# Optimization experiments

Measured on AMD Instinct MI355X. Metric: run time of the kernel, lower is better.

## Reference

```python
import jax, jax.numpy as jnp
import numpy as np

WS, SHIFT = 4, 2
Z, H, W = 16, 32, 32
C, HEADS, MLP = 384, 12, 1536
B = 4
N = WS ** 3                      # tokens per 3D window = 64
NW = (Z // WS) * (H // WS) * (W // WS)  # windows per sample = 256
L = Z * H * W
HEAD_DIM = C // HEADS


def _rel_pos_index():
    # replicates meshgrid_3d (which reverses its args) + index arithmetic
    arrs = (np.arange(WS), np.arange(WS), np.arange(WS))  # already symmetric (cubic)
    grids = []
    for i in range(3):
        slc = [1, 1, 1]; slc[i] = WS
        a = arrs[i].reshape(slc)
        for j in range(3):
            if j != i:
                a = a.repeat(WS, axis=j)
        grids.append(a)
    coords = np.stack(grids).reshape(3, -1)            # [3, N]
    rel = coords[:, :, None] - coords[:, None, :]      # [3, N, N]
    rel = rel.transpose(1, 2, 0)                       # [N, N, 3]
    rel[:, :, 0] += WS - 1
    rel[:, :, 1] += WS - 1
    rel[:, :, 2] += WS - 1
    rel[:, :, 0] *= (2 * WS - 1) * (2 * WS - 1)
    rel[:, :, 1] *= 2 * WS - 1
    return rel.sum(-1)                                 # [N, N] ints in [0, (2ws-1)^3)


def _attn_mask():
    # shifted-window mask, exactly as in build()
    m = np.zeros((Z, H, W))
    sl = (slice(0, -WS), slice(-WS, -SHIFT), slice(-SHIFT, None))
    cnt = 0
    for z in sl:
        for h in sl:
            for w in sl:
                m[z, h, w] = cnt
                cnt += 1
    mw = m.reshape(Z // WS, WS, H // WS, WS, W // WS, WS)
    mw = mw.transpose(0, 2, 4, 1, 3, 5).reshape(-1, N)        # [nW, N]
    diff = mw[:, None, :] - mw[:, :, None]                    # [nW, N, N]
    return np.where(diff != 0, -100.0, 0.0).astype(np.float32)


REL_IDX = jnp.asarray(_rel_pos_index())
MASK = jnp.asarray(_attn_mask())


def _ln(x, g, b):
    mu = jnp.mean(x, -1, keepdims=True)
    var = jnp.mean((x - mu) ** 2, -1, keepdims=True)
    return (x - mu) / jnp.sqrt(var + 1e-5) * g + b


def setup_inputs() -> dict:
    key = jax.random.key(0)
    ks = jax.random.split(key, 16)
    s = 0.02
    return {
        "x": jax.random.normal(ks[0], (B, L, C), jnp.float32),
        "norm1_g": jnp.ones((C,), jnp.float32),
        "norm1_b": jnp.zeros((C,), jnp.float32),
        "qkv_w": jax.random.normal(ks[1], (C, 3 * C), jnp.float32) * s,
        "qkv_b": jnp.zeros((3 * C,), jnp.float32),
        "proj_w": jax.random.normal(ks[2], (C, C), jnp.float32) * s,
        "proj_b": jnp.zeros((C,), jnp.float32),
        "rel_bias": jax.random.normal(ks[3], ((2 * WS - 1) ** 3, HEADS), jnp.float32) * s,
        "norm2_g": jnp.ones((C,), jnp.float32),
        "norm2_b": jnp.zeros((C,), jnp.float32),
        "fc1_w": jax.random.normal(ks[4], (C, MLP), jnp.float32) * s,
        "fc1_b": jnp.zeros((MLP,), jnp.float32),
        "fc2_w": jax.random.normal(ks[5], (MLP, C), jnp.float32) * s,
        "fc2_b": jnp.zeros((C,), jnp.float32),
    }


def reference(x, norm1_g, norm1_b, qkv_w, qkv_b, proj_w, proj_b, rel_bias,
              norm2_g, norm2_b, fc1_w, fc1_b, fc2_w, fc2_b):
    b = x.shape[0]
    skip = x
    h = _ln(x, norm1_g, norm1_b).reshape(b, Z, H, W, C)
    h = jnp.roll(h, (-SHIFT, -SHIFT, -SHIFT), axis=(1, 2, 3))
    # window partition -> [b*nW, N, C]
    win = h.reshape(b, Z // WS, WS, H // WS, WS, W // WS, WS, C)
    win = win.transpose(0, 1, 3, 5, 2, 4, 6, 7).reshape(-1, N, C)
    # windowed multi-head attention
    qkv = (win @ qkv_w + qkv_b).reshape(-1, N, 3, HEADS, HEAD_DIM)
    qkv = qkv.transpose(2, 0, 3, 1, 4)                        # [3, bnW, h, N, d]
    q, k, v = qkv[0], qkv[1], qkv[2]
    scale = HEAD_DIM ** -0.5
    attn = jnp.einsum('whnd,whmd->whnm', q * scale, k)        # [bnW, h, N, N]
    bias = rel_bias[REL_IDX.reshape(-1)].reshape(N, N, HEADS).transpose(2, 0, 1)
    attn = attn + bias[None]
    attn = attn.reshape(b, NW, HEADS, N, N) + MASK[None, :, None]
    attn = jax.nn.softmax(attn, axis=-1).reshape(-1, HEADS, N, N)
    o = jnp.einsum('whnm,whmd->whnd', attn, v)
    o = o.transpose(0, 2, 1, 3).reshape(-1, N, C) @ proj_w + proj_b
    # window reverse + unshift
    o = o.reshape(b, Z // WS, H // WS, W // WS, WS, WS, WS, C)
    o = o.transpose(0, 1, 4, 2, 5, 3, 6, 7).reshape(b, Z, H, W, C)
    o = jnp.roll(o, (SHIFT, SHIFT, SHIFT), axis=(1, 2, 3)).reshape(b, L, C)
    x2 = skip + o
    m = _ln(x2, norm2_g, norm2_b)
    m = jax.nn.gelu(m @ fc1_w + fc1_b, approximate=False) @ fc2_w + fc2_b
    return x2 + m
```

## Files before the change

### kernel.cpp

```cpp
#include <hip/hip_runtime.h>
#include <hip/hip_bf16.h>
#include <cstdint>
#include <cmath>


typedef __attribute__((ext_vector_type(4))) float f32x4;
typedef __attribute__((ext_vector_type(8))) __bf16 bf16x8_t;

static __device__ __forceinline__ short f2bf(float f) {
  unsigned u = __builtin_bit_cast(unsigned, f);
  unsigned lsb = (u >> 16) & 1u;
  u += 0x7fffu + lsb;
  return (short)(u >> 16);
}

static __device__ __forceinline__ void gload_lds16(const short* g, short* l) {
  __builtin_amdgcn_global_load_lds(
      (const __attribute__((address_space(1))) void*)g,
      (__attribute__((address_space(3))) void*)l, 16, 0, 0);
}

static constexpr size_t OFF_Q    = 0;
static constexpr size_t OFF_K    = 50331648;
static constexpr size_t OFF_V    = 100663296;
static constexpr size_t OFF_HID  = 0;
static constexpr size_t OFF_WIN  = 201326592;
static constexpr size_t OFF_WQ   = OFF_WIN + 50331648;
static constexpr size_t OFF_WP   = OFF_WQ  + 884736;
static constexpr size_t OFF_W1   = OFF_WP  + 294912;
static constexpr size_t OFF_W2   = OFF_W1  + 1179648;

__global__ void k_w2bf_t(const float* __restrict__ w, short* __restrict__ wt,
                         int K, int N) {
  int idx = blockIdx.x * 256 + threadIdx.x;
  if (idx >= K * N) return;
  int k = idx / N, n = idx - k * N;
  wt[(size_t)n * K + k] = f2bf(w[idx]);
}

__global__ __launch_bounds__(256) void k_ln1_window(
    const float* __restrict__ x, const float* __restrict__ gw,
    const float* __restrict__ gb, short* __restrict__ win) {
  int slot = blockIdx.x * 4 + (threadIdx.x >> 6);
  int lane = threadIdx.x & 63;
  int widx = slot >> 6, n = slot & 63;
  int bidx = widx >> 8, wloc = widx & 255;
  int z = ((wloc >> 6) << 2) + (n >> 4);
  int h = (((wloc >> 3) & 7) << 2) + ((n >> 2) & 3);
  int w = ((wloc & 7) << 2) + (n & 3);
  int zs = (z + 2) & 15, hs = (h + 2) & 31, ws = (w + 2) & 31;
  const float* xp = x + ((size_t)bidx * 16384 + zs * 1024 + hs * 32 + ws) * 384;
  float2 u[3]; float s = 0.f, s2 = 0.f;
#pragma unroll
  for (int j = 0; j < 3; j++) {
    u[j] = *(const float2*)(xp + lane * 2 + j * 128);
    s += u[j].x + u[j].y; s2 += u[j].x * u[j].x + u[j].y * u[j].y;
  }
#pragma unroll
  for (int o = 1; o < 64; o <<= 1) { s += __shfl_xor(s, o); s2 += __shfl_xor(s2, o); }
  float mu = s * (1.f / 384.f);
  float rinv = rsqrtf(s2 * (1.f / 384.f) - mu * mu + 1e-5f);
  short* wp = win + (size_t)slot * 384;
#pragma unroll
  for (int j = 0; j < 3; j++) {
    int c = lane * 2 + j * 128;
    ushort2 o;
    o.x = (unsigned short)f2bf((u[j].x - mu) * rinv * gw[c] + gb[c]);
    o.y = (unsigned short)f2bf((u[j].y - mu) * rinv * gw[c + 1] + gb[c + 1]);
    *(ushort2*)(wp + c) = o;
  }
}

__global__ __launch_bounds__(256) void k_ln2(
    const float* __restrict__ x2, const float* __restrict__ gw,
    const float* __restrict__ gb, short* __restrict__ h2) {
  int t = blockIdx.x * 4 + (threadIdx.x >> 6);
  int lane = threadIdx.x & 63;
  const float* xp = x2 + (size_t)t * 384;
  float2 u[3]; float s = 0.f, s2 = 0.f;
#pragma unroll
  for (int j = 0; j < 3; j++) {
    u[j] = *(const float2*)(xp + lane * 2 + j * 128);
    s += u[j].x + u[j].y; s2 += u[j].x * u[j].x + u[j].y * u[j].y;
  }
#pragma unroll
  for (int o = 1; o < 64; o <<= 1) { s += __shfl_xor(s, o); s2 += __shfl_xor(s2, o); }
  float mu = s * (1.f / 384.f);
  float rinv = rsqrtf(s2 * (1.f / 384.f) - mu * mu + 1e-5f);
  short* hp = h2 + (size_t)t * 384;
#pragma unroll
  for (int j = 0; j < 3; j++) {
    int c = lane * 2 + j * 128;
    ushort2 o;
    o.x = (unsigned short)f2bf((u[j].x - mu) * rinv * gw[c] + gb[c]);
    o.y = (unsigned short)f2bf((u[j].y - mu) * rinv * gw[c + 1] + gb[c + 1]);
    *(ushort2*)(hp + c) = o;
  }
}

template <int EPI, int KDIM>
__global__ __launch_bounds__(256) void k_gemm(
    const short* __restrict__ A, const short* __restrict__ Bt,
    const float* __restrict__ bias, short* __restrict__ ob0,
    short* __restrict__ ob1, short* __restrict__ ob2,
    const float* __restrict__ aux, float* __restrict__ of32) {
  __shared__ short As[16384];
  __shared__ short Bs[16384];
  const int tid = threadIdx.x;
  const int wave = tid >> 6, lane = tid & 63;
  const int g = lane >> 4, li = lane & 15;

  const int nx = gridDim.x;
  const int nwg = nx * gridDim.y;
  int bid = blockIdx.y * nx + blockIdx.x;
  const int cpx = nwg >> 3;
  bid = (bid & 7) * cpx + (bid >> 3);
  const int m0 = (bid / nx) << 7, n0 = (bid % nx) << 7;

  const int srow = tid >> 3;
  const int sc8 = (tid & 7) ^ (srow & 7);
  const short* gA = A + (size_t)(m0 + srow) * KDIM + sc8 * 8;
  const short* gB = Bt + (size_t)(n0 + srow) * KDIM + sc8 * 8;
  short* lA = As + wave * 512;
  short* lB = Bs + wave * 512;

  const int wm = wave >> 1, wn = wave & 1;
  const int kx = (li & 7) << 3;
  const short* ra = As + (wm * 64 + li) * 64;
  const short* rb = Bs + (wn * 64 + li) * 64;
  const int c00 = (g * 8) ^ kx;
  const int c32 = (32 + g * 8) ^ kx;

  f32x4 acc[4][4] = {};

#define STAGE(buf, kt)                                                        \
  do {                                                                        \
    _Pragma("unroll") for (int p = 0; p < 4; p++) {                           \
      gload_lds16(gA + (size_t)(p * 32) * KDIM + (kt),                        \
                  lA + (buf) * 8192 + p * 2048);                              \
      gload_lds16(gB + (size_t)(p * 32) * KDIM + (kt),                        \
                  lB + (buf) * 8192 + p * 2048);                              \
    }                                                                         \
  } while (0)

#define COMPUTE(buf)                                                          \
  do {                                                                        \
    const short* ra_ = ra + (buf) * 8192;                                     \
    const short* rb_ = rb + (buf) * 8192;                                     \
    bf16x8_t a0[4], a1[4], b0[4], b1[4];                                      \
    _Pragma("unroll") for (int i = 0; i < 4; i++) {                           \
      a0[i] = *(const bf16x8_t*)(ra_ + i * 1024 + c00);                       \
      a1[i] = *(const bf16x8_t*)(ra_ + i * 1024 + c32);                       \
      b0[i] = *(const bf16x8_t*)(rb_ + i * 1024 + c00);                       \
      b1[i] = *(const bf16x8_t*)(rb_ + i * 1024 + c32);                       \
    }                                                                         \
    _Pragma("unroll") for (int mi = 0; mi < 4; mi++)                          \
        _Pragma("unroll") for (int ni = 0; ni < 4; ni++) acc[mi][ni] =        \
        __builtin_amdgcn_mfma_f32_16x16x32_bf16(a0[mi], b0[ni], acc[mi][ni],  \
                                                0, 0, 0);                     \
    _Pragma("unroll") for (int mi = 0; mi < 4; mi++)                          \
        _Pragma("unroll") for (int ni = 0; ni < 4; ni++) acc[mi][ni] =        \
        __builtin_amdgcn_mfma_f32_16x16x32_bf16(a1[mi], b1[ni], acc[mi][ni],  \
                                                0, 0, 0);                     \
  } while (0)

  constexpr int NT = KDIM / 64;
  STAGE(0, 0);
  asm volatile("s_waitcnt vmcnt(0)" ::: "memory");
  __syncthreads();
  int cur = 0;
  for (int t = 0; t < NT - 1; ++t) {
    STAGE(cur ^ 1, (t + 1) * 64);
    COMPUTE(cur);
    asm volatile("s_waitcnt vmcnt(0)" ::: "memory");
    __syncthreads();
    cur ^= 1;
  }
  COMPUTE(cur);
#undef STAGE
#undef COMPUTE

#pragma unroll
  for (int mi = 0; mi < 4; mi++) {
#pragma unroll
    for (int ni = 0; ni < 4; ni++) {
      const int col = n0 + wn * 64 + ni * 16 + li;
      const float bc = bias[col];
      const int rbase = m0 + wm * 64 + mi * 16 + g * 4;
      if constexpr (EPI == 0) {
        const int s = col / 384;
        const int rem = col - s * 384;
        const int head = rem >> 5, d = rem & 31;
#pragma unroll
        for (int r = 0; r < 4; r++) {
          const int row = rbase + r;
          const int widx = row >> 6, n = row & 63;
          float v = acc[mi][ni][r] + bc;
          if (s == 0)
            ob0[(((size_t)widx * 12 + head) * 64 + n) * 32 + d] =
                f2bf(v * 0.17677669529663687f);
          else if (s == 1)
            ob1[(((size_t)widx * 12 + head) * 64 + n) * 32 + d] = f2bf(v);
          else
            ob2[(((size_t)widx * 12 + head) * 32 + d) * 64 + n] = f2bf(v);
        }
      } else if constexpr (EPI == 1) {
#pragma unroll
        for (int r = 0; r < 4; r++) {
          const int row = rbase + r;
          const int widx = row >> 6, n = row & 63;
          const int wloc = widx & 255, bb = widx >> 8;
          const int z = ((wloc >> 6) << 2) + (n >> 4);
          const int h = (((wloc >> 3) & 7) << 2) + ((n >> 2) & 3);
          const int w = ((wloc & 7) << 2) + (n & 3);
          const int zs = (z + 2) & 15, hs = (h + 2) & 31, wsx = (w + 2) & 31;
          const size_t t = (size_t)bb * 16384 + zs * 1024 + hs * 32 + wsx;
          of32[t * 384 + col] = aux[t * 384 + col] + acc[mi][ni][r] + bc;
        }
      } else if constexpr (EPI == 2) {
#pragma unroll
        for (int r = 0; r < 4; r++) {
          const int row = rbase + r;
          float v = acc[mi][ni][r] + bc;
          ob0[(size_t)row * 1536 + col] =
              f2bf(0.5f * v * (1.f + erff(v * 0.70710678118654752f)));
        }
      } else {
#pragma unroll
        for (int r = 0; r < 4; r++) {
          const int row = rbase + r;
          of32[(size_t)row * 384 + col] =
              aux[(size_t)row * 384 + col] + acc[mi][ni][r] + bc;
        }
      }
    }
  }
}

__global__ __launch_bounds__(256) void k_attn(
    const short* __restrict__ qb, const short* __restrict__ kb,
    const short* __restrict__ vb, const float* __restrict__ relb,
    short* __restrict__ owin) {
  __shared__ short pt[4][5120];
  const int wave = threadIdx.x >> 6;
  const int wh_ = blockIdx.x * 4 + wave;
  const int widx = wh_ / 12, head = wh_ - widx * 12;
  const int lane = threadIdx.x & 63;
  const int g = lane >> 4, li = lane & 15;
  const short* qp = qb + (size_t)wh_ * 2048;
  const short* kp = kb + (size_t)wh_ * 2048;
  const short* vp = vb + (size_t)wh_ * 2048;
  short* ptw = pt[wave];
  bf16x8_t kf[4], qf[4];
#pragma unroll
  for (int t = 0; t < 4; t++) {
    kf[t] = *(const bf16x8_t*)(kp + (t * 16 + li) * 32 + g * 8);
    qf[t] = *(const bf16x8_t*)(qp + (t * 16 + li) * 32 + g * 8);
  }
  f32x4 zero = {0.f, 0.f, 0.f, 0.f};
  f32x4 st[4][4];
#pragma unroll
  for (int ti = 0; ti < 4; ti++)
#pragma unroll
    for (int tj = 0; tj < 4; tj++)
      st[ti][tj] = __builtin_amdgcn_mfma_f32_16x16x32_bf16(kf[ti], qf[tj], zero, 0, 0, 0);
  const int wloc = widx & 255;
  const int wz = wloc >> 6, wh2 = (wloc >> 3) & 7, ww2 = wloc & 7;
#pragma unroll
  for (int tj = 0; tj < 4; tj++) {
    const int qn = tj * 16 + li;
    const int qz = qn >> 4, qh = (qn >> 2) & 3, qw = qn & 3;
    const int cq = ((wz < 3) ? 0 : ((qz < 2) ? 1 : 2)) * 9 +
                   ((wh2 < 7) ? 0 : ((qh < 2) ? 1 : 2)) * 3 +
                   ((ww2 < 7) ? 0 : ((qw < 2) ? 1 : 2));
    float mx = -1e30f;
#pragma unroll
    for (int ti = 0; ti < 4; ti++) {
#pragma unroll
      for (int r = 0; r < 4; r++) {
        const int kn = ti * 16 + g * 4 + r;
        const int kz = kn >> 4, kh = (kn >> 2) & 3, kw = kn & 3;
        const int ck = ((wz < 3) ? 0 : ((kz < 2) ? 1 : 2)) * 9 +
                       ((wh2 < 7) ? 0 : ((kh < 2) ? 1 : 2)) * 3 +
                       ((ww2 < 7) ? 0 : ((kw < 2) ? 1 : 2));
        const int idx = (qz - kz + 3) * 49 + (qh - kh + 3) * 7 + (qw - kw + 3);
        float v = st[ti][tj][r] + relb[idx * 12 + head] + ((ck == cq) ? 0.f : -100.f);
        st[ti][tj][r] = v;
        mx = fmaxf(mx, v);
      }
    }
    mx = fmaxf(mx, __shfl_xor(mx, 16));
    mx = fmaxf(mx, __shfl_xor(mx, 32));
    float sum = 0.f;
#pragma unroll
    for (int ti = 0; ti < 4; ti++)
#pragma unroll
      for (int r = 0; r < 4; r++) {
        float e = __expf(st[ti][tj][r] - mx);
        st[ti][tj][r] = e;
        sum += e;
      }
    sum += __shfl_xor(sum, 16);
    sum += __shfl_xor(sum, 32);
    const float rs = 1.f / sum;
#pragma unroll
    for (int ti = 0; ti < 4; ti++)
#pragma unroll
      for (int r = 0; r < 4; r++)
        ptw[qn * 80 + ti * 16 + g * 4 + r] = f2bf(st[ti][tj][r] * rs);
  }
  __syncthreads();
  f32x4 o[4][2] = {};
#pragma unroll
  for (int kb2 = 0; kb2 < 2; kb2++) {
    bf16x8_t pa[4], bv[2];
#pragma unroll
    for (int tq = 0; tq < 4; tq++)
      pa[tq] = *(const bf16x8_t*)(ptw + (tq * 16 + li) * 80 + kb2 * 32 + g * 8);
#pragma unroll
    for (int td = 0; td < 2; td++)
      bv[td] = *(const bf16x8_t*)(vp + (td * 16 + li) * 64 + kb2 * 32 + g * 8);
#pragma unroll
    for (int tq = 0; tq < 4; tq++)
#pragma unroll
      for (int td = 0; td < 2; td++)
        o[tq][td] = __builtin_amdgcn_mfma_f32_16x16x32_bf16(pa[tq], bv[td], o[tq][td], 0, 0, 0);
  }
#pragma unroll
  for (int tq = 0; tq < 4; tq++)
#pragma unroll
    for (int td = 0; td < 2; td++)
#pragma unroll
      for (int r = 0; r < 4; r++) {
        const int qn = tq * 16 + g * 4 + r;
        const int d = td * 16 + li;
        owin[((size_t)widx * 64 + qn) * 384 + head * 32 + d] = f2bf(o[tq][td][r]);
      }
}

extern "C" void kernel_launch(void* const* d_in, const int* in_sizes, int n_in,
                              void* d_out, int out_size, void* d_ws,
                              size_t ws_size, hipStream_t stream) {
  (void)in_sizes; (void)n_in; (void)out_size; (void)ws_size;
  const float* x      = (const float*)d_in[0];
  const float* n1g    = (const float*)d_in[1];
  const float* n1b    = (const float*)d_in[2];
  const float* qkv_w  = (const float*)d_in[3];
  const float* qkv_b  = (const float*)d_in[4];
  const float* proj_w = (const float*)d_in[5];
  const float* proj_b = (const float*)d_in[6];
  const float* relb   = (const float*)d_in[7];
  const float* n2g    = (const float*)d_in[8];
  const float* n2b    = (const float*)d_in[9];
  const float* fc1_w  = (const float*)d_in[10];
  const float* fc1_b  = (const float*)d_in[11];
  const float* fc2_w  = (const float*)d_in[12];
  const float* fc2_b  = (const float*)d_in[13];
  float* out = (float*)d_out;
  char* ws = (char*)d_ws;

  short* qbuf = (short*)(ws + OFF_Q);
  short* kbuf = (short*)(ws + OFF_K);
  short* vbuf = (short*)(ws + OFF_V);
  short* hid  = (short*)(ws + OFF_HID);
  short* win  = (short*)(ws + OFF_WIN);
  short* owin = (short*)(ws + OFF_WIN);
  short* h2   = (short*)(ws + OFF_WIN);
  float* x2   = out;
  short* wq   = (short*)(ws + OFF_WQ);
  short* wp   = (short*)(ws + OFF_WP);
  short* w1   = (short*)(ws + OFF_W1);
  short* w2   = (short*)(ws + OFF_W2);

  k_w2bf_t<<<(384 * 1152 + 255) / 256, 256, 0, stream>>>(qkv_w, wq, 384, 1152);
  k_w2bf_t<<<(384 * 384 + 255) / 256, 256, 0, stream>>>(proj_w, wp, 384, 384);
  k_w2bf_t<<<(384 * 1536 + 255) / 256, 256, 0, stream>>>(fc1_w, w1, 384, 1536);
  k_w2bf_t<<<(1536 * 384 + 255) / 256, 256, 0, stream>>>(fc2_w, w2, 1536, 384);

  k_ln1_window<<<16384, 256, 0, stream>>>(x, n1g, n1b, win);
  k_gemm<0, 384><<<dim3(9, 512), 256, 0, stream>>>(win, wq, qkv_b, qbuf, kbuf,
                                                   vbuf, nullptr, nullptr);
  k_attn<<<3072, 256, 0, stream>>>(qbuf, kbuf, vbuf, relb, owin);
  k_gemm<1, 384><<<dim3(3, 512), 256, 0, stream>>>(owin, wp, proj_b, nullptr,
                                                   nullptr, nullptr, x, x2);
  k_ln2<<<16384, 256, 0, stream>>>(x2, n2g, n2b, h2);
  k_gemm<2, 384><<<dim3(12, 512), 256, 0, stream>>>(h2, w1, fc1_b, hid, nullptr,
                                                    nullptr, nullptr, nullptr);
  k_gemm<3, 1536><<<dim3(3, 512), 256, 0, stream>>>(hid, w2, fc2_b, nullptr,
                                                    nullptr, nullptr, x2, out);
}
```

Measured before the change: 805.0 us.

## Halve GEMM K-tile, swizzle LDS layout, stage V via LDS, approximate GELU

The GEMM K-step drops from 64 to 32, halving LDS use so three workgroups can fit per CU (launch_bounds 3). The LDS row layout and swizzle are rebuilt, and the loop is restructured with split barriers and a partial vmcnt wait. The V-transpose epilogue of the QKV GEMM now goes through LDS for coalesced 16-byte stores. Exact erf GELU is replaced by a sigmoid-style exp2 approximation, which trades some accuracy for fewer instructions. The weight-convert kernel is also templated on its dimensions.

```diff
diff --git a/kernel.cpp b/kernel.cpp
--- a/kernel.cpp
+++ b/kernel.cpp
@@ -5,6 +5,7 @@
 
 
 typedef __attribute__((ext_vector_type(4))) float f32x4;
+typedef __attribute__((ext_vector_type(4))) int i32x4;
 typedef __attribute__((ext_vector_type(8))) __bf16 bf16x8_t;
 
 static __device__ __forceinline__ short f2bf(float f) {
@@ -12,6 +13,13 @@
   unsigned lsb = (u >> 16) & 1u;
   u += 0x7fffu + lsb;
   return (short)(u >> 16);
+}
+
+static __device__ __forceinline__ float fgelu(float x) {
+  float xx = x * x;
+  float p = __builtin_fmaf(-0.102944499f, xx, -2.302118131f);
+  float e = __builtin_amdgcn_exp2f(p * x);
+  return x * __builtin_amdgcn_rcpf(1.f + e);
 }
 
 static __device__ __forceinline__ void gload_lds16(const short* g, short* l) {
@@ -30,8 +38,8 @@
 static constexpr size_t OFF_W1   = OFF_WP  + 294912;
 static constexpr size_t OFF_W2   = OFF_W1  + 1179648;
 
-__global__ void k_w2bf_t(const float* __restrict__ w, short* __restrict__ wt,
-                         int K, int N) {
+template <int K, int N>
+__global__ void k_w2bf_t(const float* __restrict__ w, short* __restrict__ wt) {
   int idx = blockIdx.x * 256 + threadIdx.x;
   if (idx >= K * N) return;
   int k = idx / N, n = idx - k * N;
@@ -99,16 +107,17 @@
 }
 
 template <int EPI, int KDIM>
-__global__ __launch_bounds__(256) void k_gemm(
+__global__ __launch_bounds__(256, 3) void k_gemm(
     const short* __restrict__ A, const short* __restrict__ Bt,
     const float* __restrict__ bias, short* __restrict__ ob0,
     short* __restrict__ ob1, short* __restrict__ ob2,
     const float* __restrict__ aux, float* __restrict__ of32) {
-  __shared__ short As[16384];
-  __shared__ short Bs[16384];
+  __shared__ short smem[16384];
+  short* As = smem;
+  short* Bs = smem + 8192;
   const int tid = threadIdx.x;
   const int wave = tid >> 6, lane = tid & 63;
-  const int g = lane >> 4, li = lane & 15;
+  const int g = lane >> 4, li = lane & 15, li2 = li >> 1;
 
   const int nx = gridDim.x;
   const int nwg = nx * gridDim.y;
@@ -117,120 +126,162 @@
   bid = (bid & 7) * cpx + (bid >> 3);
   const int m0 = (bid / nx) << 7, n0 = (bid % nx) << 7;
 
-  const int srow = tid >> 3;
-  const int sc8 = (tid & 7) ^ (srow & 7);
-  const short* gA = A + (size_t)(m0 + srow) * KDIM + sc8 * 8;
-  const short* gB = Bt + (size_t)(n0 + srow) * KDIM + sc8 * 8;
+  const int hi = lane >> 3, lo = lane & 7;
+  const int su = lo ^ hi;
+  const int srow = hi * 2 + (su >> 2);
+  const int scol = (su & 3) << 3;
+  const short* gA = A + (size_t)(m0 + wave * 16 + srow) * KDIM + scol;
+  const short* gB = Bt + (size_t)(n0 + wave * 16 + srow) * KDIM + scol;
   short* lA = As + wave * 512;
   short* lB = Bs + wave * 512;
 
   const int wm = wave >> 1, wn = wave & 1;
-  const int kx = (li & 7) << 3;
-  const short* ra = As + (wm * 64 + li) * 64;
-  const short* rb = Bs + (wn * 64 + li) * 64;
-  const int c00 = (g * 8) ^ kx;
-  const int c32 = (32 + g * 8) ^ kx;
+  const int slot = ((((li & 1) << 2) + g) ^ li2) << 3;
+  const int abase = (wm * 32 + li2) * 64 + slot;
+  const int bbase = (wn * 32 + li2) * 64 + slot;
 
   f32x4 acc[4][4] = {};
 
 #define STAGE(buf, kt)                                                        \
   do {                                                                        \
-    _Pragma("unroll") for (int p = 0; p < 4; p++) {                           \
-      gload_lds16(gA + (size_t)(p * 32) * KDIM + (kt),                        \
-                  lA + (buf) * 8192 + p * 2048);                              \
-      gload_lds16(gB + (size_t)(p * 32) * KDIM + (kt),                        \
-                  lB + (buf) * 8192 + p * 2048);                              \
-    }                                                                         \
+    gload_lds16(gA + (kt), lA + (buf) * 4096);                                \
+    gload_lds16(gA + (size_t)64 * KDIM + (kt), lA + (buf) * 4096 + 2048);     \
+    gload_lds16(gB + (kt), lB + (buf) * 4096);                                \
+    gload_lds16(gB + (size_t)64 * KDIM + (kt), lB + (buf) * 4096 + 2048);     \
   } while (0)
 
 #define COMPUTE(buf)                                                          \
   do {                                                                        \
-    const short* ra_ = ra + (buf) * 8192;                                     \
-    const short* rb_ = rb + (buf) * 8192;                                     \
-    bf16x8_t a0[4], a1[4], b0[4], b1[4];                                      \
+    const short* pa = As + (buf) * 4096 + abase;                              \
+    const short* pb = Bs + (buf) * 4096 + bbase;                              \
+    bf16x8_t a[4], b[4];                                                      \
     _Pragma("unroll") for (int i = 0; i < 4; i++) {                           \
-      a0[i] = *(const bf16x8_t*)(ra_ + i * 1024 + c00);                       \
-      a1[i] = *(const bf16x8_t*)(ra_ + i * 1024 + c32);                       \
-      b0[i] = *(const bf16x8_t*)(rb_ + i * 1024 + c00);                       \
-      b1[i] = *(const bf16x8_t*)(rb_ + i * 1024 + c32);                       \
+      a[i] = *(const bf16x8_t*)(pa + i * 512);                                \
+      b[i] = *(const bf16x8_t*)(pb + i * 512);                                \
     }                                                                         \
     _Pragma("unroll") for (int mi = 0; mi < 4; mi++)                          \
         _Pragma("unroll") for (int ni = 0; ni < 4; ni++) acc[mi][ni] =        \
-        __builtin_amdgcn_mfma_f32_16x16x32_bf16(a0[mi], b0[ni], acc[mi][ni],  \
-                                                0, 0, 0);                     \
-    _Pragma("unroll") for (int mi = 0; mi < 4; mi++)                          \
-        _Pragma("unroll") for (int ni = 0; ni < 4; ni++) acc[mi][ni] =        \
-        __builtin_amdgcn_mfma_f32_16x16x32_bf16(a1[mi], b1[ni], acc[mi][ni],  \
+        __builtin_amdgcn_mfma_f32_16x16x32_bf16(a[mi], b[ni], acc[mi][ni],    \
                                                 0, 0, 0);                     \
   } while (0)
 
-  constexpr int NT = KDIM / 64;
+  constexpr int NT = KDIM / 32;
   STAGE(0, 0);
-  asm volatile("s_waitcnt vmcnt(0)" ::: "memory");
-  __syncthreads();
-  int cur = 0;
-  for (int t = 0; t < NT - 1; ++t) {
-    STAGE(cur ^ 1, (t + 1) * 64);
-    COMPUTE(cur);
-    asm volatile("s_waitcnt vmcnt(0)" ::: "memory");
-    __syncthreads();
-    cur ^= 1;
-  }
-  COMPUTE(cur);
+#pragma unroll 2
+  for (int t = 0; t < NT; ++t) {
+    asm volatile("s_waitcnt lgkmcnt(0)" ::: "memory");
+    __builtin_amdgcn_s_barrier();
+    if (t + 1 < NT) {
+      STAGE((t + 1) & 1, (t + 1) * 32);
+      asm volatile("s_waitcnt vmcnt(4)" ::: "memory");
+    } else {
+      asm volatile("s_waitcnt vmcnt(0)" ::: "memory");
+    }
+    __builtin_amdgcn_s_barrier();
+    COMPUTE(t & 1);
+  }
 #undef STAGE
 #undef COMPUTE
 
-#pragma unroll
-  for (int mi = 0; mi < 4; mi++) {
-#pragma unroll
-    for (int ni = 0; ni < 4; ni++) {
-      const int col = n0 + wn * 64 + ni * 16 + li;
-      const float bc = bias[col];
-      const int rbase = m0 + wm * 64 + mi * 16 + g * 4;
-      if constexpr (EPI == 0) {
-        const int s = col / 384;
-        const int rem = col - s * 384;
-        const int head = rem >> 5, d = rem & 31;
+  if constexpr (EPI == 0) {
+    const int s = n0 / 384;
+    const int nloc = n0 % 384;
+    if (s < 2) {
+      short* dst = (s == 0) ? ob0 : ob1;
+      const float scale = (s == 0) ? 0.17677669529663687f : 1.f;
+#pragma unroll
+      for (int mi = 0; mi < 4; mi++) {
+#pragma unroll
+        for (int ni = 0; ni < 4; ni++) {
+          const int colc = wn * 64 + ni * 16 + li;
+          const float bc = bias[n0 + colc];
+          const int head = (nloc + colc) >> 5, d = colc & 31;
+#pragma unroll
+          for (int r = 0; r < 4; r++) {
+            const int row = m0 + wm * 64 + mi * 16 + g * 4 + r;
+            const int widx = row >> 6, n = row & 63;
+            dst[(((size_t)widx * 12 + head) * 64 + n) * 32 + d] =
+                f2bf((acc[mi][ni][r] + bc) * scale);
+          }
+        }
+      }
+    } else {
+      __syncthreads();
+      short* ct = smem;
+#pragma unroll
+      for (int mi = 0; mi < 4; mi++) {
+#pragma unroll
+        for (int ni = 0; ni < 4; ni++) {
+          const int colc = wn * 64 + ni * 16 + li;
+          const float bc = bias[n0 + colc];
+          const int hh = colc >> 5, d = colc & 31;
+#pragma unroll
+          for (int r = 0; r < 4; r++) {
+            const int rowloc = wm * 64 + mi * 16 + g * 4 + r;
+            const int wl = rowloc >> 6, n = rowloc & 63;
+            int idx16 = (wl * 4 + hh) * 256 + d * 8 + (n >> 3);
+            idx16 ^= (idx16 >> 3) & 7;
+            ct[idx16 * 8 + (n & 7)] = f2bf(acc[mi][ni][r] + bc);
+          }
+        }
+      }
+      __syncthreads();
+      const int hb = nloc >> 5;
+      const int wg0 = m0 >> 6;
+#pragma unroll
+      for (int k2 = 0; k2 < 8; k2++) {
+        const int c = k2 * 256 + tid;
+        const int cs = c ^ ((c >> 3) & 7);
+        i32x4 val = *(const i32x4*)(ct + cs * 8);
+        const int run = c >> 8, sub2 = c & 255;
+        short* gp = ob2 +
+                    ((size_t)(wg0 + (run >> 2)) * 12 + hb + (run & 3)) * 2048 +
+                    sub2 * 8;
+        *(i32x4*)gp = val;
+      }
+    }
+  } else if constexpr (EPI == 2) {
+#pragma unroll
+    for (int mi = 0; mi < 4; mi++) {
+#pragma unroll
+      for (int ni = 0; ni < 4; ni++) {
+        const int col = n0 + wn * 64 + ni * 16 + li;
+        const float bc = bias[col];
 #pragma unroll
         for (int r = 0; r < 4; r++) {
-          const int row = rbase + r;
-          const int widx = row >> 6, n = row & 63;
-          float v = acc[mi][ni][r] + bc;
-          if (s == 0)
-            ob0[(((size_t)widx * 12 + head) * 64 + n) * 32 + d] =
-                f2bf(v * 0.17677669529663687f);
-          else if (s == 1)
-            ob1[(((size_t)widx * 12 + head) * 64 + n) * 32 + d] = f2bf(v);
-          else
-            ob2[(((size_t)widx * 12 + head) * 32 + d) * 64 + n] = f2bf(v);
+          const int row = m0 + wm * 64 + mi * 16 + g * 4 + r;
+          ob0[(size_t)row * 1536 + col] = f2bf(fgelu(acc[mi][ni][r] + bc));
         }
-      } else if constexpr (EPI == 1) {
-#pragma unroll
-        for (int r = 0; r < 4; r++) {
-          const int row = rbase + r;
-          const int widx = row >> 6, n = row & 63;
-          const int wloc = widx & 255, bb = widx >> 8;
-          const int z = ((wloc >> 6) << 2) + (n >> 4);
-          const int h = (((wloc >> 3) & 7) << 2) + ((n >> 2) & 3);
-          const int w = ((wloc & 7) << 2) + (n & 3);
-          const int zs = (z + 2) & 15, hs = (h + 2) & 31, wsx = (w + 2) & 31;
-          const size_t t = (size_t)bb * 16384 + zs * 1024 + hs * 32 + wsx;
-          of32[t * 384 + col] = aux[t * 384 + col] + acc[mi][ni][r] + bc;
-        }
-      } else if constexpr (EPI == 2) {
-#pragma unroll
-        for (int r = 0; r < 4; r++) {
-          const int row = rbase + r;
-          float v = acc[mi][ni][r] + bc;
-          ob0[(size_t)row * 1536 + col] =
-              f2bf(0.5f * v * (1.f + erff(v * 0.70710678118654752f)));
-        }
-      } else {
-#pragma unroll
-        for (int r = 0; r < 4; r++) {
-          const int row = rbase + r;
-          of32[(size_t)row * 384 + col] =
-              aux[(size_t)row * 384 + col] + acc[mi][ni][r] + bc;
+      }
+    }
+  } else {
+#pragma unroll
+    for (int mi = 0; mi < 4; mi++) {
+#pragma unroll
+      for (int ni = 0; ni < 4; ni++) {
+        const int col = n0 + wn * 64 + ni * 16 + li;
+        const float bc = bias[col];
+        const int rbase = m0 + wm * 64 + mi * 16 + g * 4;
+        if constexpr (EPI == 1) {
+#pragma unroll
+          for (int r = 0; r < 4; r++) {
+            const int row = rbase + r;
+            const int widx = row >> 6, n = row & 63;
+            const int wloc = widx & 255, bb = widx >> 8;
+            const int z = ((wloc >> 6) << 2) + (n >> 4);
+            const int h = (((wloc >> 3) & 7) << 2) + ((n >> 2) & 3);
+            const int w = ((wloc & 7) << 2) + (n & 3);
+            const int zs = (z + 2) & 15, hs = (h + 2) & 31, wsx = (w + 2) & 31;
+            const size_t t = (size_t)bb * 16384 + zs * 1024 + hs * 32 + wsx;
+            of32[t * 384 + col] = aux[t * 384 + col] + acc[mi][ni][r] + bc;
+          }
+        } else {
+#pragma unroll
+          for (int r = 0; r < 4; r++) {
+            const int row = rbase + r;
+            of32[(size_t)row * 384 + col] =
+                aux[(size_t)row * 384 + col] + acc[mi][ni][r] + bc;
+          }
         }
       }
     }
@@ -372,10 +423,10 @@
   short* w1   = (short*)(ws + OFF_W1);
   short* w2   = (short*)(ws + OFF_W2);
 
-  k_w2bf_t<<<(384 * 1152 + 255) / 256, 256, 0, stream>>>(qkv_w, wq, 384, 1152);
-  k_w2bf_t<<<(384 * 384 + 255) / 256, 256, 0, stream>>>(proj_w, wp, 384, 384);
-  k_w2bf_t<<<(384 * 1536 + 255) / 256, 256, 0, stream>>>(fc1_w, w1, 384, 1536);
-  k_w2bf_t<<<(1536 * 384 + 255) / 256, 256, 0, stream>>>(fc2_w, w2, 1536, 384);
+  k_w2bf_t<384, 1152><<<(384 * 1152 + 255) / 256, 256, 0, stream>>>(qkv_w, wq);
+  k_w2bf_t<384, 384><<<(384 * 384 + 255) / 256, 256, 0, stream>>>(proj_w, wp);
+  k_w2bf_t<384, 1536><<<(384 * 1536 + 255) / 256, 256, 0, stream>>>(fc1_w, w1);
+  k_w2bf_t<1536, 384><<<(1536 * 384 + 255) / 256, 256, 0, stream>>>(fc2_w, w2);
 
   k_ln1_window<<<16384, 256, 0, stream>>>(x, n1g, n1b, win);
   k_gemm<0, 384><<<dim3(9, 512), 256, 0, stream>>>(win, wq, qkv_b, qbuf, kbuf,
```

Result: faster. 683.6 us (-15.1%).
